# Kernel optimization log

Measured on AMD Instinct MI355X. Metric: run time of the kernel, lower is better.

Reference implementation:

```python
import jax, jax.numpy as jnp
import numpy as np

N = 16384
F_IN = 256
F_OUT = 256


def setup_inputs() -> dict:
    key = jax.random.key(0)
    k1, k2, k3 = jax.random.split(key, 3)
    x = jax.random.normal(k1, (N, F_IN), dtype=jnp.float32)
    # dense 0/1 adjacency (original masks with adj[j] == 1)
    adj = jax.random.randint(k2, (N, N), 0, 2, dtype=jnp.int32)
    # glorot-uniform init for weight [2F_in, F_out]
    stdv = np.sqrt(6.0 / (2 * F_IN + F_OUT)).astype(np.float32)
    weight = jax.random.uniform(k3, (2 * F_IN, F_OUT), dtype=jnp.float32,
                                minval=-stdv, maxval=stdv)
    bias = jnp.zeros((F_OUT,), dtype=jnp.float32)
    return {"x": x, "adj": adj, "weight": weight, "bias": bias}


def reference(x, adj, weight, bias):
    # Mean over neighbors (adj row == 1): segment-mean expressed as a
    # normalized dense matmul -- equivalent to the per-row boolean-mask mean.
    a = adj.astype(x.dtype)                      # [N, N]
    deg = jnp.sum(a, axis=1, keepdims=True)      # [N, 1]
    x1 = (a @ x) / deg                           # [N, F] neighbor mean
    n_x = jnp.concatenate([x1, x], axis=1)       # [N, 2F]
    return n_x @ weight + bias                   # [N, F_out]
```

## Files before the change

### kernel.cpp

```cpp
#include <hip/hip_runtime.h>
#include <hip/hip_bf16.h>
#include <stdint.h>


typedef short bf16x8 __attribute__((ext_vector_type(8)));
typedef float f32x4  __attribute__((ext_vector_type(4)));

__device__ __forceinline__ uint32_t pack_bf16_rne(float lo, float hi) {
    uint32_t ul = __float_as_uint(lo);
    uint32_t uh = __float_as_uint(hi);
    ul = (ul + 0x7fffu + ((ul >> 16) & 1u)) >> 16;
    uh = (uh + 0x7fffu + ((uh >> 16) & 1u)) >> 16;
    return ul | (uh << 16);
}

__device__ __forceinline__ void gload_lds16(const void* g, void* l) {
    __builtin_amdgcn_global_load_lds(
        (__attribute__((address_space(1))) void*)g,
        (__attribute__((address_space(3))) void*)l, 16, 0, 0);
}

__global__ __launch_bounds__(256) void k_transpose_w(const float* __restrict__ w,
                                                     uint16_t* __restrict__ wt) {
    int idx = blockIdx.x * 256 + threadIdx.x;
    int n = idx >> 8;
    int k = idx & 255;
    int row = (n < 256) ? k : (256 + k);
    int col = (n < 256) ? n : (n - 256);
    uint32_t u = __float_as_uint(w[row * 256 + col]);
    u = (u + 0x7fffu + ((u >> 16) & 1u)) >> 16;
    wt[idx] = (uint16_t)u;
}

__global__ __launch_bounds__(256) void k_small_gemm(const float* __restrict__ x,
                                                    const uint16_t* __restrict__ wt,
                                                    const float* __restrict__ bias,
                                                    uint16_t* __restrict__ yT,
                                                    float* __restrict__ z) {
    __shared__ uint16_t As[128 * 32];
    __shared__ uint16_t Bs[128 * 32];

    const int t  = threadIdx.x;
    const int ct = blockIdx.x;
    const int rt = blockIdx.y;
    const int m0 = rt * 128;
    const int n0 = ct * 128;

    const int lane = t & 63, w = t >> 6;
    const int wr = w >> 1, wc = w & 1;
    const int l15 = lane & 15, quad = lane >> 4;

    f32x4 acc[4][4] = {};

    float4 a_reg[4];
    uint4  b_reg[2];

#pragma unroll
    for (int i = 0; i < 4; ++i) {
        int f4 = t + 256 * i, row = f4 >> 3, c4 = f4 & 7;
        a_reg[i] = *(const float4*)(x + (m0 + row) * 256 + c4 * 4);
    }
#pragma unroll
    for (int i = 0; i < 2; ++i) {
        int u4 = t + 256 * i, n_l = u4 >> 2, part = u4 & 3;
        b_reg[i] = *(const uint4*)(wt + (n0 + n_l) * 256 + part * 8);
    }

    for (int kk = 0; kk < 8; ++kk) {
        __syncthreads();
#pragma unroll
        for (int i = 0; i < 4; ++i) {
            int f4 = t + 256 * i, row = f4 >> 3, c4 = f4 & 7;
            uint2 p;
            p.x = pack_bf16_rne(a_reg[i].x, a_reg[i].y);
            p.y = pack_bf16_rne(a_reg[i].z, a_reg[i].w);
            *(uint2*)(As + row * 32 + c4 * 4) = p;
        }
#pragma unroll
        for (int i = 0; i < 2; ++i) {
            int u4 = t + 256 * i, n_l = u4 >> 2, part = u4 & 3;
            *(uint4*)(Bs + n_l * 32 + part * 8) = b_reg[i];
        }
        if (kk < 7) {
            int k0 = (kk + 1) * 32;
#pragma unroll
            for (int i = 0; i < 4; ++i) {
                int f4 = t + 256 * i, row = f4 >> 3, c4 = f4 & 7;
                a_reg[i] = *(const float4*)(x + (m0 + row) * 256 + k0 + c4 * 4);
            }
#pragma unroll
            for (int i = 0; i < 2; ++i) {
                int u4 = t + 256 * i, n_l = u4 >> 2, part = u4 & 3;
                b_reg[i] = *(const uint4*)(wt + (n0 + n_l) * 256 + k0 + part * 8);
            }
        }
        __syncthreads();

        bf16x8 a_frag[4], b_frag[4];
#pragma unroll
        for (int fr = 0; fr < 4; ++fr)
            a_frag[fr] = *(const bf16x8*)(As + (wr * 64 + fr * 16 + l15) * 32 + quad * 8);
#pragma unroll
        for (int fc = 0; fc < 4; ++fc)
            b_frag[fc] = *(const bf16x8*)(Bs + (wc * 64 + fc * 16 + l15) * 32 + quad * 8);
#pragma unroll
        for (int fr = 0; fr < 4; ++fr)
#pragma unroll
            for (int fc = 0; fc < 4; ++fc)
                acc[fr][fc] = __builtin_amdgcn_mfma_f32_16x16x32_bf16(
                    a_frag[fr], b_frag[fc], acc[fr][fc], 0, 0, 0);
    }

    if (ct < 2) {
#pragma unroll
        for (int fr = 0; fr < 4; ++fr) {
            int m_base = m0 + wr * 64 + fr * 16 + quad * 4;
#pragma unroll
            for (int fc = 0; fc < 4; ++fc) {
                int n_g = n0 + wc * 64 + fc * 16 + l15;
                uint2 pp;
                pp.x = pack_bf16_rne(acc[fr][fc][0], acc[fr][fc][1]);
                pp.y = pack_bf16_rne(acc[fr][fc][2], acc[fr][fc][3]);
                *(uint2*)(yT + (size_t)n_g * 16384 + m_base) = pp;
            }
        }
    } else {
#pragma unroll
        for (int fr = 0; fr < 4; ++fr) {
            int m_base = m0 + wr * 64 + fr * 16 + quad * 4;
#pragma unroll
            for (int fc = 0; fc < 4; ++fc) {
                int n_g = (n0 - 256) + wc * 64 + fc * 16 + l15;
                float bv = bias[n_g];
#pragma unroll
                for (int r = 0; r < 4; ++r)
                    z[(size_t)(m_base + r) * 256 + n_g] = acc[fr][fc][r] + bv;
            }
        }
    }
}

#define A_STRIDE 40
#define A_SZ (64 * A_STRIDE)
#define B_SZ (256 * 32)
#define KITER 256

#define BIG_STEP(CONS, PACK, ISSUE, KK)                                         \
  do {                                                                          \
    int4 aNew = aB;                                                             \
    if ((KK) < KITER - 2) {                                                     \
      aNew = pa4[0]; pa4 += 8;                                                  \
      gload_lds16(pbg0, Bs##ISSUE + b_lb0); pbg0 += 32;                         \
      gload_lds16(pbg1, Bs##ISSUE + b_lb1); pbg1 += 32;                         \
    }                                                                           \
       \
    asm volatile("s_waitcnt vmcnt(3)" ::: "memory");                            \
    if ((KK) < KITER - 1) {                                                     \
      degp += aB.x + aB.y + aB.z + aB.w;                                        \
      uint2 pv;                                                                 \
      pv.x = (uint32_t)(aB.x | (aB.y << 16)) * 0x3F80u;                         \
      pv.y = (uint32_t)(aB.z | (aB.w << 16)) * 0x3F80u;                         \
      *(uint2*)&As##PACK[a_lds] = pv;                                           \
      aB = aNew;                                                                \
    }                                                                           \
    {                                                                           \
      bf16x8 af[2], bfr[4];                                                     \
      _Pragma("unroll") for (int fr = 0; fr < 2; ++fr) {                        \
        int row = wr * 32 + fr * 16 + l15;                                      \
        af[fr] = *(const bf16x8*)(As##CONS + row * A_STRIDE + quad * 8);        \
      }                                                                         \
      _Pragma("unroll") for (int fc = 0; fc < 4; ++fc) {                        \
        int n = wc * 64 + fc * 16 + l15;                                        \
        int cs = quad ^ ((n >> 1) & 3);                                         \
        bfr[fc] = *(const bf16x8*)(Bs##CONS + n * 32 + cs * 8);                 \
      }                                                                         \
      _Pragma("unroll") for (int fr = 0; fr < 2; ++fr)                          \
        _Pragma("unroll") for (int fc = 0; fc < 4; ++fc)                        \
          acc[fr][fc] = __builtin_amdgcn_mfma_f32_16x16x32_bf16(                \
              af[fr], bfr[fc], acc[fr][fc], 0, 0, 0);                           \
    }                                                                           \
                             \
    asm volatile("s_waitcnt lgkmcnt(0)\n\ts_barrier" ::: "memory");             \
  } while (0)

__global__ __launch_bounds__(512, 4) void k_big_gemm(const int* __restrict__ adj,
                                                     const uint16_t* __restrict__ yT,
                                                     float* __restrict__ part,
                                                     int* __restrict__ degw) {
    __shared__ uint16_t As0[A_SZ], As1[A_SZ], As2[A_SZ];
    __shared__ uint16_t Bs0[B_SZ], Bs1[B_SZ], Bs2[B_SZ];

    const int t = threadIdx.x;
    const int m0 = blockIdx.x * 64;
    const int ky = blockIdx.y;
    const int kbase = ky * 8192;
    const int lane = t & 63, w = t >> 6;
    const int wr = w >> 2, wc = w & 3;
    const int l15 = lane & 15, quad = lane >> 4;

    f32x4 acc[2][4] = {};

    const int a_n = t >> 3, a_c4 = t & 7;
    const int4* pa4 = (const int4*)(adj + (size_t)(m0 + a_n) * 16384 + kbase) + a_c4;
    const int a_lds = a_n * A_STRIDE + a_c4 * 4;

    const uint16_t *pbg0, *pbg1;
    int b_lb0, b_lb1;
    {
        int base0 = (w * 2 + 0) * 64, base1 = (w * 2 + 1) * 64;
        int s0 = base0 + lane, s1 = base1 + lane;
        int bn0 = s0 >> 2, bn1 = s1 >> 2;
        int bc0 = (s0 & 3) ^ ((bn0 >> 1) & 3);
        int bc1 = (s1 & 3) ^ ((bn1 >> 1) & 3);
        pbg0 = yT + (size_t)bn0 * 16384 + kbase + bc0 * 8;
        pbg1 = yT + (size_t)bn1 * 16384 + kbase + bc1 * 8;
        b_lb0 = base0 * 8;
        b_lb1 = base1 * 8;
    }

    gload_lds16(pbg0, Bs0 + b_lb0); pbg0 += 32;
    gload_lds16(pbg1, Bs0 + b_lb1); pbg1 += 32;
    int4 a0 = pa4[0];
    gload_lds16(pbg0, Bs1 + b_lb0); pbg0 += 32;
    gload_lds16(pbg1, Bs1 + b_lb1); pbg1 += 32;
    int4 aB = pa4[8];
    pa4 += 16;
    asm volatile("s_waitcnt vmcnt(2)" ::: "memory");
    int degp = a0.x + a0.y + a0.z + a0.w;
    {
        uint2 pv;
        pv.x = (uint32_t)(a0.x | (a0.y << 16)) * 0x3F80u;
        pv.y = (uint32_t)(a0.z | (a0.w << 16)) * 0x3F80u;
        *(uint2*)&As0[a_lds] = pv;
    }
    asm volatile("s_waitcnt lgkmcnt(0)\n\ts_barrier" ::: "memory");

    for (int kk = 0; kk < KITER - 1; kk += 3) {
        BIG_STEP(0, 1, 2, kk);
        BIG_STEP(1, 2, 0, kk + 1);
        BIG_STEP(2, 0, 1, kk + 2);
    }
    BIG_STEP(0, 1, 2, KITER - 1);

    degp += __shfl_down(degp, 4);
    degp += __shfl_down(degp, 2);
    degp += __shfl_down(degp, 1);
    if ((t & 7) == 0) degw[ky * 16384 + m0 + a_n] = degp;

    float* pc = part + (size_t)ky * 16384 * 256;
#pragma unroll
    for (int fr = 0; fr < 2; ++fr) {
#pragma unroll
        for (int r = 0; r < 4; ++r) {
            int m_l = wr * 32 + fr * 16 + quad * 4 + r;
            size_t mrow = (size_t)(m0 + m_l) * 256;
#pragma unroll
            for (int fc = 0; fc < 4; ++fc) {
                int n_g = wc * 64 + fc * 16 + l15;
                pc[mrow + n_g] = acc[fr][fc][r];
            }
        }
    }
}

__global__ __launch_bounds__(256) void k_reduce(const float* __restrict__ part,
                                                const int* __restrict__ degw,
                                                const float* __restrict__ z,
                                                float* __restrict__ out) {
    int i4 = blockIdx.x * 256 + threadIdx.x;
    int m = i4 >> 6;
    float4 p0 = ((const float4*)part)[i4];
    float4 p1 = ((const float4*)part)[i4 + 16384 * 64];
    float4 zz = ((const float4*)z)[i4];
    float inv = 1.0f / (float)(degw[m] + degw[16384 + m]);
    float4 o;
    o.x = (p0.x + p1.x) * inv + zz.x;
    o.y = (p0.y + p1.y) * inv + zz.y;
    o.z = (p0.z + p1.z) * inv + zz.z;
    o.w = (p0.w + p1.w) * inv + zz.w;
    ((float4*)out)[i4] = o;
}

extern "C" void kernel_launch(void* const* d_in, const int* in_sizes, int n_in,
                              void* d_out, int out_size, void* d_ws, size_t ws_size,
                              hipStream_t stream) {
    const float* x      = (const float*)d_in[0];
    const int*   adj    = (const int*)d_in[1];
    const float* weight = (const float*)d_in[2];
    const float* bias   = (const float*)d_in[3];
    float* out = (float*)d_out;

    uint16_t* wt   = (uint16_t*)d_ws;
    uint16_t* yT   = (uint16_t*)((char*)d_ws + 262144);
    float*    z    = (float*)((char*)d_ws + 262144 + 8388608);
    float*    partb= (float*)((char*)d_ws + 262144 + 8388608 + 16777216);
    int*      degw = (int*)((char*)d_ws + 262144 + 8388608 + 16777216 + 33554432);

    k_transpose_w<<<512, 256, 0, stream>>>(weight, wt);
    k_small_gemm<<<dim3(4, 128), 256, 0, stream>>>(x, wt, bias, yT, z);
    k_big_gemm<<<dim3(256, 2), 512, 0, stream>>>(adj, yT, partb, degw);
    k_reduce<<<4096, 256, 0, stream>>>(partb, degw, z, out);
}
```

Baseline: 1.501 ms.

## Bit-pack adjacency in a pre-pass and feed bits to the big GEMM

Adds a kernel that reads the int32 adjacency once, packs it into 64-bit ballot masks and computes row degrees with popcount. The big GEMM then reads 32-bit words of bits instead of int4 vectors and expands them to bf16 ones/zeros in LDS, and no longer reduces degrees itself. Both approaches read the full 1 GiB adjacency once, so total HBM traffic changes little. The extra kernel launch and its serial dependency may offset whatever the smaller A-stream in the GEMM saves.

```diff
diff --git a/kernel.cpp b/kernel.cpp
--- a/kernel.cpp
+++ b/kernel.cpp
@@ -18,6 +18,28 @@
     __builtin_amdgcn_global_load_lds(
         (__attribute__((address_space(1))) void*)g,
         (__attribute__((address_space(3))) void*)l, 16, 0, 0);
+}
+
+__global__ __launch_bounds__(256) void k_bitpack(const int* __restrict__ adj,
+                                                 unsigned long long* __restrict__ bits,
+                                                 int* __restrict__ deg) {
+    __shared__ int ds[4];
+    const int row = blockIdx.x, t = threadIdx.x, lane = t & 63, w = t >> 6;
+    const int* p = adj + (size_t)row * 16384 + w * 64 + lane;
+    unsigned long long* brow = bits + (size_t)row * 256 + w;
+    int dpop = 0;
+#pragma unroll 4
+    for (int it = 0; it < 64; ++it) {
+        int v = p[it * 256];
+        unsigned long long m = __ballot(v != 0);
+        if (lane == 0) {
+            brow[it * 4] = m;
+            dpop += __popcll(m);
+        }
+    }
+    if (lane == 0) ds[w] = dpop;
+    __syncthreads();
+    if (t == 0) deg[row] = ds[0] + ds[1] + ds[2] + ds[3];
 }
 
 __global__ __launch_bounds__(256) void k_transpose_w(const float* __restrict__ w,
@@ -147,21 +169,20 @@
 
 #define BIG_STEP(CONS, PACK, ISSUE, KK)                                         \
   do {                                                                          \
-    int4 aNew = aB;                                                             \
     if ((KK) < KITER - 2) {                                                     \
-      aNew = pa4[0]; pa4 += 8;                                                  \
       gload_lds16(pbg0, Bs##ISSUE + b_lb0); pbg0 += 32;                         \
       gload_lds16(pbg1, Bs##ISSUE + b_lb1); pbg1 += 32;                         \
     }                                                                           \
-       \
+    uint32_t wNew = wB;                                                         \
+    if ((KK) < KITER - 2) wNew = pw[(KK) + 2] >> a_sh;                          \
+     \
     asm volatile("s_waitcnt vmcnt(3)" ::: "memory");                            \
     if ((KK) < KITER - 1) {                                                     \
-      degp += aB.x + aB.y + aB.z + aB.w;                                        \
       uint2 pv;                                                                 \
-      pv.x = (uint32_t)(aB.x | (aB.y << 16)) * 0x3F80u;                         \
-      pv.y = (uint32_t)(aB.z | (aB.w << 16)) * 0x3F80u;                         \
+      pv.x = (wB & 1u) * 0x3F80u + ((wB >> 1) & 1u) * 0x3F800000u;              \
+      pv.y = ((wB >> 2) & 1u) * 0x3F80u + ((wB >> 3) & 1u) * 0x3F800000u;       \
       *(uint2*)&As##PACK[a_lds] = pv;                                           \
-      aB = aNew;                                                                \
+      wB = wNew;                                                                \
     }                                                                           \
     {                                                                           \
       bf16x8 af[2], bfr[4];                                                     \
@@ -179,14 +200,12 @@
           acc[fr][fc] = __builtin_amdgcn_mfma_f32_16x16x32_bf16(                \
               af[fr], bfr[fc], acc[fr][fc], 0, 0, 0);                           \
     }                                                                           \
-                             \
     asm volatile("s_waitcnt lgkmcnt(0)\n\ts_barrier" ::: "memory");             \
   } while (0)
 
-__global__ __launch_bounds__(512, 4) void k_big_gemm(const int* __restrict__ adj,
+__global__ __launch_bounds__(512, 4) void k_big_gemm(const uint32_t* __restrict__ bits32,
                                                      const uint16_t* __restrict__ yT,
-                                                     float* __restrict__ part,
-                                                     int* __restrict__ degw) {
+                                                     float* __restrict__ part) {
     __shared__ uint16_t As0[A_SZ], As1[A_SZ], As2[A_SZ];
     __shared__ uint16_t Bs0[B_SZ], Bs1[B_SZ], Bs2[B_SZ];
 
@@ -201,7 +220,8 @@
     f32x4 acc[2][4] = {};
 
     const int a_n = t >> 3, a_c4 = t & 7;
-    const int4* pa4 = (const int4*)(adj + (size_t)(m0 + a_n) * 16384 + kbase) + a_c4;
+    const int a_sh = a_c4 * 4;
+    const uint32_t* pw = bits32 + (size_t)(m0 + a_n) * 512 + ky * 256;
     const int a_lds = a_n * A_STRIDE + a_c4 * 4;
 
     const uint16_t *pbg0, *pbg1;
@@ -220,19 +240,17 @@
 
     gload_lds16(pbg0, Bs0 + b_lb0); pbg0 += 32;
     gload_lds16(pbg1, Bs0 + b_lb1); pbg1 += 32;
-    int4 a0 = pa4[0];
+    uint32_t w0 = pw[0] >> a_sh;
     gload_lds16(pbg0, Bs1 + b_lb0); pbg0 += 32;
     gload_lds16(pbg1, Bs1 + b_lb1); pbg1 += 32;
-    int4 aB = pa4[8];
-    pa4 += 16;
-    asm volatile("s_waitcnt vmcnt(2)" ::: "memory");
-    int degp = a0.x + a0.y + a0.z + a0.w;
+    uint32_t wB = pw[1] >> a_sh;
     {
         uint2 pv;
-        pv.x = (uint32_t)(a0.x | (a0.y << 16)) * 0x3F80u;
-        pv.y = (uint32_t)(a0.z | (a0.w << 16)) * 0x3F80u;
+        pv.x = (w0 & 1u) * 0x3F80u + ((w0 >> 1) & 1u) * 0x3F800000u;
+        pv.y = ((w0 >> 2) & 1u) * 0x3F80u + ((w0 >> 3) & 1u) * 0x3F800000u;
         *(uint2*)&As0[a_lds] = pv;
     }
+    asm volatile("s_waitcnt vmcnt(3)" ::: "memory");
     asm volatile("s_waitcnt lgkmcnt(0)\n\ts_barrier" ::: "memory");
 
     for (int kk = 0; kk < KITER - 1; kk += 3) {
@@ -242,11 +260,6 @@
     }
     BIG_STEP(0, 1, 2, KITER - 1);
 
-    degp += __shfl_down(degp, 4);
-    degp += __shfl_down(degp, 2);
-    degp += __shfl_down(degp, 1);
-    if ((t & 7) == 0) degw[ky * 16384 + m0 + a_n] = degp;
-
     float* pc = part + (size_t)ky * 16384 * 256;
 #pragma unroll
     for (int fr = 0; fr < 2; ++fr) {
@@ -264,7 +277,7 @@
 }
 
 __global__ __launch_bounds__(256) void k_reduce(const float* __restrict__ part,
-                                                const int* __restrict__ degw,
+                                                const int* __restrict__ deg,
                                                 const float* __restrict__ z,
                                                 float* __restrict__ out) {
     int i4 = blockIdx.x * 256 + threadIdx.x;
@@ -272,7 +285,7 @@
     float4 p0 = ((const float4*)part)[i4];
     float4 p1 = ((const float4*)part)[i4 + 16384 * 64];
     float4 zz = ((const float4*)z)[i4];
-    float inv = 1.0f / (float)(degw[m] + degw[16384 + m]);
+    float inv = 1.0f / (float)deg[m];
     float4 o;
     o.x = (p0.x + p1.x) * inv + zz.x;
     o.y = (p0.y + p1.y) * inv + zz.y;
@@ -290,14 +303,18 @@
     const float* bias   = (const float*)d_in[3];
     float* out = (float*)d_out;
 
-    uint16_t* wt   = (uint16_t*)d_ws;
-    uint16_t* yT   = (uint16_t*)((char*)d_ws + 262144);
-    float*    z    = (float*)((char*)d_ws + 262144 + 8388608);
-    float*    partb= (float*)((char*)d_ws + 262144 + 8388608 + 16777216);
-    int*      degw = (int*)((char*)d_ws + 262144 + 8388608 + 16777216 + 33554432);
-
+    char* wsb = (char*)d_ws;
+    uint16_t* wt   = (uint16_t*)(wsb);
+    uint16_t* yT   = (uint16_t*)(wsb + 262144);
+    float*    z    = (float*)(wsb + 262144 + 8388608);
+    float*    partb= (float*)(wsb + 262144 + 8388608 + 16777216);
+    int*      deg  = (int*)(wsb + 262144 + 8388608 + 16777216 + 33554432);
+    unsigned long long* bits =
+        (unsigned long long*)(wsb + 262144 + 8388608 + 16777216 + 33554432 + 65536);
+
+    k_bitpack<<<16384, 256, 0, stream>>>(adj, bits, deg);
     k_transpose_w<<<512, 256, 0, stream>>>(weight, wt);
     k_small_gemm<<<dim3(4, 128), 256, 0, stream>>>(x, wt, bias, yT, z);
-    k_big_gemm<<<dim3(256, 2), 512, 0, stream>>>(adj, yT, partb, degw);
-    k_reduce<<<4096, 256, 0, stream>>>(partb, degw, z, out);
-}
+    k_big_gemm<<<dim3(256, 2), 512, 0, stream>>>((const uint32_t*)bits, yT, partb);
+    k_reduce<<<4096, 256, 0, stream>>>(partb, deg, z, out);
+}
```

After: 1.663 ms. +10.8%, slower.

## Tile yT into contiguous k-chunks and stage B through registers instead of LDS-DMA

Applied to the files above, without the earlier changes.

Intermediate yT is now stored in a tiled layout: for each 32-wide k chunk, all 256 features sit contiguously, so each k-step's B tile is one contiguous 16 KB block. The big GEMM drops the direct global-to-LDS loads. It prefetches B and A into registers two to three steps ahead and writes them to padded LDS (stride 36, no XOR swizzle). The aim is fully coalesced B reads with deeper prefetch. The cost is more register pressure and extra VGPR-to-LDS write instructions.

```diff
diff --git a/kernel.cpp b/kernel.cpp
--- a/kernel.cpp
+++ b/kernel.cpp
@@ -12,12 +12,6 @@
     ul = (ul + 0x7fffu + ((ul >> 16) & 1u)) >> 16;
     uh = (uh + 0x7fffu + ((uh >> 16) & 1u)) >> 16;
     return ul | (uh << 16);
-}
-
-__device__ __forceinline__ void gload_lds16(const void* g, void* l) {
-    __builtin_amdgcn_global_load_lds(
-        (__attribute__((address_space(1))) void*)g,
-        (__attribute__((address_space(3))) void*)l, 16, 0, 0);
 }
 
 __global__ __launch_bounds__(256) void k_transpose_w(const float* __restrict__ w,
@@ -35,7 +29,7 @@
 __global__ __launch_bounds__(256) void k_small_gemm(const float* __restrict__ x,
                                                     const uint16_t* __restrict__ wt,
                                                     const float* __restrict__ bias,
-                                                    uint16_t* __restrict__ yT,
+                                                    uint16_t* __restrict__ yTt,
                                                     float* __restrict__ z) {
     __shared__ uint16_t As[128 * 32];
     __shared__ uint16_t Bs[128 * 32];
@@ -121,7 +115,7 @@
                 uint2 pp;
                 pp.x = pack_bf16_rne(acc[fr][fc][0], acc[fr][fc][1]);
                 pp.y = pack_bf16_rne(acc[fr][fc][2], acc[fr][fc][3]);
-                *(uint2*)(yT + (size_t)n_g * 16384 + m_base) = pp;
+                *(uint2*)(yTt + (size_t)(m_base >> 5) * 8192 + n_g * 32 + (m_base & 31)) = pp;
             }
         }
     } else {
@@ -140,51 +134,53 @@
     }
 }
 
-#define A_STRIDE 40
+#define A_STRIDE 36
+#define B_STRIDE 36
 #define A_SZ (64 * A_STRIDE)
-#define B_SZ (256 * 32)
+#define B_SZ (256 * B_STRIDE)
 #define KITER 256
 
-#define BIG_STEP(CONS, PACK, ISSUE, KK)                                         \
+#define STEP(ARD, BRD, AWR, BWR, KK)                                            \
   do {                                                                          \
-    int4 aNew = aB;                                                             \
-    if ((KK) < KITER - 2) {                                                     \
-      aNew = pa4[0]; pa4 += 8;                                                  \
-      gload_lds16(pbg0, Bs##ISSUE + b_lb0); pbg0 += 32;                         \
-      gload_lds16(pbg1, Bs##ISSUE + b_lb1); pbg1 += 32;                         \
+    if ((KK) < KITER - 2) {                                   \
+      bN0 = *(const uint4*)(pB);                                                \
+      bN1 = *(const uint4*)(pB + 4096);                                         \
+      pB += 8192;                                                               \
     }                                                                           \
-       \
-    asm volatile("s_waitcnt vmcnt(3)" ::: "memory");                            \
-    if ((KK) < KITER - 1) {                                                     \
-      degp += aB.x + aB.y + aB.z + aB.w;                                        \
+    if ((KK) < KITER - 3) {                                   \
+      aN = pa4[0]; pa4 += 8;                                                    \
+    }                                                                           \
+    if ((KK) < KITER - 1) {                              \
+      degp += aQ0.x + aQ0.y + aQ0.z + aQ0.w;                                    \
       uint2 pv;                                                                 \
-      pv.x = (uint32_t)(aB.x | (aB.y << 16)) * 0x3F80u;                         \
-      pv.y = (uint32_t)(aB.z | (aB.w << 16)) * 0x3F80u;                         \
-      *(uint2*)&As##PACK[a_lds] = pv;                                           \
-      aB = aNew;                                                                \
+      pv.x = (uint32_t)(aQ0.x | (aQ0.y << 16)) * 0x3F80u;                       \
+      pv.y = (uint32_t)(aQ0.z | (aQ0.w << 16)) * 0x3F80u;                       \
+      *(uint2*)&As##AWR[a_lds] = pv;                                            \
+      *(uint4*)&Bs##BWR[b_lds0] = bC0;                                          \
+      *(uint4*)&Bs##BWR[b_lds1] = bC1;                                          \
     }                                                                           \
     {                                                                           \
       bf16x8 af[2], bfr[4];                                                     \
       _Pragma("unroll") for (int fr = 0; fr < 2; ++fr) {                        \
         int row = wr * 32 + fr * 16 + l15;                                      \
-        af[fr] = *(const bf16x8*)(As##CONS + row * A_STRIDE + quad * 8);        \
+        af[fr] = *(const bf16x8*)(As##ARD + row * A_STRIDE + quad * 8);         \
       }                                                                         \
       _Pragma("unroll") for (int fc = 0; fc < 4; ++fc) {                        \
         int n = wc * 64 + fc * 16 + l15;                                        \
-        int cs = quad ^ ((n >> 1) & 3);                                         \
-        bfr[fc] = *(const bf16x8*)(Bs##CONS + n * 32 + cs * 8);                 \
+        bfr[fc] = *(const bf16x8*)(Bs##BRD + n * B_STRIDE + quad * 8);          \
       }                                                                         \
       _Pragma("unroll") for (int fr = 0; fr < 2; ++fr)                          \
         _Pragma("unroll") for (int fc = 0; fc < 4; ++fc)                        \
           acc[fr][fc] = __builtin_amdgcn_mfma_f32_16x16x32_bf16(                \
               af[fr], bfr[fc], acc[fr][fc], 0, 0, 0);                           \
     }                                                                           \
-                             \
+    aQ0 = aQ1; aQ1 = aQ2; aQ2 = aN;                                             \
+    bC0 = bN0; bC1 = bN1;                                                       \
     asm volatile("s_waitcnt lgkmcnt(0)\n\ts_barrier" ::: "memory");             \
   } while (0)
 
 __global__ __launch_bounds__(512, 4) void k_big_gemm(const int* __restrict__ adj,
-                                                     const uint16_t* __restrict__ yT,
+                                                     const uint16_t* __restrict__ yTt,
                                                      float* __restrict__ part,
                                                      int* __restrict__ degw) {
     __shared__ uint16_t As0[A_SZ], As1[A_SZ], As2[A_SZ];
@@ -193,7 +189,6 @@
     const int t = threadIdx.x;
     const int m0 = blockIdx.x * 64;
     const int ky = blockIdx.y;
-    const int kbase = ky * 8192;
     const int lane = t & 63, w = t >> 6;
     const int wr = w >> 2, wc = w & 3;
     const int l15 = lane & 15, quad = lane >> 4;
@@ -201,46 +196,48 @@
     f32x4 acc[2][4] = {};
 
     const int a_n = t >> 3, a_c4 = t & 7;
-    const int4* pa4 = (const int4*)(adj + (size_t)(m0 + a_n) * 16384 + kbase) + a_c4;
+    const int4* pa4 = (const int4*)(adj + (size_t)(m0 + a_n) * 16384 + ky * 8192) + a_c4;
     const int a_lds = a_n * A_STRIDE + a_c4 * 4;
 
-    const uint16_t *pbg0, *pbg1;
-    int b_lb0, b_lb1;
-    {
-        int base0 = (w * 2 + 0) * 64, base1 = (w * 2 + 1) * 64;
-        int s0 = base0 + lane, s1 = base1 + lane;
-        int bn0 = s0 >> 2, bn1 = s1 >> 2;
-        int bc0 = (s0 & 3) ^ ((bn0 >> 1) & 3);
-        int bc1 = (s1 & 3) ^ ((bn1 >> 1) & 3);
-        pbg0 = yT + (size_t)bn0 * 16384 + kbase + bc0 * 8;
-        pbg1 = yT + (size_t)bn1 * 16384 + kbase + bc1 * 8;
-        b_lb0 = base0 * 8;
-        b_lb1 = base1 * 8;
-    }
-
-    gload_lds16(pbg0, Bs0 + b_lb0); pbg0 += 32;
-    gload_lds16(pbg1, Bs0 + b_lb1); pbg1 += 32;
+    const uint16_t* pB = yTt + (size_t)(ky * 256) * 8192 + t * 8;
+    const int b_s0 = t, b_s1 = t + 512;
+    const int b_lds0 = (b_s0 >> 2) * B_STRIDE + (b_s0 & 3) * 8;
+    const int b_lds1 = (b_s1 >> 2) * B_STRIDE + (b_s1 & 3) * 8;
+
     int4 a0 = pa4[0];
-    gload_lds16(pbg0, Bs1 + b_lb0); pbg0 += 32;
-    gload_lds16(pbg1, Bs1 + b_lb1); pbg1 += 32;
-    int4 aB = pa4[8];
-    pa4 += 16;
-    asm volatile("s_waitcnt vmcnt(2)" ::: "memory");
+    int4 aQ0 = pa4[8];
+    int4 aQ1 = pa4[16];
+    int4 aQ2;
+    int4 aN = aQ1;
+    pa4 += 24;
+    uint4 b00 = *(const uint4*)(pB);
+    uint4 b01 = *(const uint4*)(pB + 4096);
+    pB += 8192;
+    uint4 bC0 = *(const uint4*)(pB);
+    uint4 bC1 = *(const uint4*)(pB + 4096);
+    pB += 8192;
+    uint4 bN0 = bC0, bN1 = bC1;
+
     int degp = a0.x + a0.y + a0.z + a0.w;
     {
         uint2 pv;
         pv.x = (uint32_t)(a0.x | (a0.y << 16)) * 0x3F80u;
         pv.y = (uint32_t)(a0.z | (a0.w << 16)) * 0x3F80u;
         *(uint2*)&As0[a_lds] = pv;
+        *(uint4*)&Bs0[b_lds0] = b00;
+        *(uint4*)&Bs0[b_lds1] = b01;
     }
     asm volatile("s_waitcnt lgkmcnt(0)\n\ts_barrier" ::: "memory");
 
-    for (int kk = 0; kk < KITER - 1; kk += 3) {
-        BIG_STEP(0, 1, 2, kk);
-        BIG_STEP(1, 2, 0, kk + 1);
-        BIG_STEP(2, 0, 1, kk + 2);
-    }
-    BIG_STEP(0, 1, 2, KITER - 1);
+    for (int kk = 0; kk < KITER - 4; kk += 3) {
+        STEP(0, 0, 1, 1, kk);
+        STEP(1, 1, 2, 2, kk + 1);
+        STEP(2, 2, 0, 0, kk + 2);
+    }
+    STEP(0, 0, 1, 1, 252);
+    STEP(1, 1, 2, 2, 253);
+    STEP(2, 2, 0, 0, 254);
+    STEP(0, 0, 1, 1, 255);
 
     degp += __shfl_down(degp, 4);
     degp += __shfl_down(degp, 2);
@@ -290,14 +287,15 @@
     const float* bias   = (const float*)d_in[3];
     float* out = (float*)d_out;
 
-    uint16_t* wt   = (uint16_t*)d_ws;
-    uint16_t* yT   = (uint16_t*)((char*)d_ws + 262144);
-    float*    z    = (float*)((char*)d_ws + 262144 + 8388608);
-    float*    partb= (float*)((char*)d_ws + 262144 + 8388608 + 16777216);
-    int*      degw = (int*)((char*)d_ws + 262144 + 8388608 + 16777216 + 33554432);
+    char* wsb = (char*)d_ws;
+    uint16_t* wt   = (uint16_t*)(wsb);
+    uint16_t* yTt  = (uint16_t*)(wsb + 262144);
+    float*    z    = (float*)(wsb + 262144 + 8388608);
+    float*    partb= (float*)(wsb + 262144 + 8388608 + 16777216);
+    int*      degw = (int*)(wsb + 262144 + 8388608 + 16777216 + 33554432);
 
     k_transpose_w<<<512, 256, 0, stream>>>(weight, wt);
-    k_small_gemm<<<dim3(4, 128), 256, 0, stream>>>(x, wt, bias, yT, z);
-    k_big_gemm<<<dim3(256, 2), 512, 0, stream>>>(adj, yT, partb, degw);
+    k_small_gemm<<<dim3(4, 128), 256, 0, stream>>>(x, wt, bias, yTt, z);
+    k_big_gemm<<<dim3(256, 2), 512, 0, stream>>>(adj, yTt, partb, degw);
     k_reduce<<<4096, 256, 0, stream>>>(partb, degw, z, out);
 }
```

After: 1.430 ms. -4.7%, faster.
